# Kernel tuning notes

Measured on AMD Instinct MI355X. Metric: run time of the kernel, lower is better.

Reference implementation:

```python
import jax, jax.numpy as jnp
import numpy as np

B, N, K = 16, 1024, 20
EPS = 1e-5

def _lin_init(key, fan_in, fan_out):
    k1, k2 = jax.random.split(key)
    s = 1.0 / np.sqrt(fan_in)
    W = jax.random.uniform(k1, (fan_in, fan_out), minval=-s, maxval=s, dtype=jnp.float32)
    b = jax.random.uniform(k2, (fan_out,), minval=-s, maxval=s, dtype=jnp.float32)
    return W, b

def setup_inputs() -> dict:
    key = jax.random.key(0)
    ks = jax.random.split(key, 12)
    pos = jax.random.normal(ks[0], (B * N, 3), dtype=jnp.float32)
    batch = jnp.repeat(jnp.arange(B, dtype=jnp.int64), N)
    W1a, b1a = _lin_init(ks[1], 6, 64);    W1b, b1b = _lin_init(ks[2], 64, 64)
    W2a, b2a = _lin_init(ks[3], 128, 64);  W2b, b2b = _lin_init(ks[4], 64, 64)
    W3a, b3a = _lin_init(ks[5], 128, 128); W3b, b3b = _lin_init(ks[6], 128, 128)
    W4a, b4a = _lin_init(ks[7], 256, 256); W4b, b4b = _lin_init(ks[8], 256, 256)
    lin1_w, lin1_b = _lin_init(ks[9], 512, 1024)
    gamma = jnp.ones((1024,), jnp.float32); beta = jnp.zeros((1024,), jnp.float32)
    lin2_w, lin2_b = _lin_init(ks[10], 1024, 40)
    return dict(pos=pos, batch=batch,
                W1a=W1a, b1a=b1a, W1b=W1b, b1b=b1b,
                W2a=W2a, b2a=b2a, W2b=W2b, b2b=b2b,
                W3a=W3a, b3a=b3a, W3b=W3b, b3b=b3b,
                W4a=W4a, b4a=b4a, W4b=W4b, b4b=b4b,
                lin1_w=lin1_w, lin1_b=lin1_b, gamma=gamma, beta=beta,
                lin2_w=lin2_w, lin2_b=lin2_b)

def _edge_conv(x, Wa, ba, Wb, bb):
    # x: [B, N, C]. Dynamic kNN in feature space (per cloud, self included,
    # matching PyG knn), edge feature [x_i, x_j - x_i], MLP, max-aggregate.
    sq = jnp.sum(x * x, axis=-1)                                   # [B,N]
    d = sq[:, :, None] - 2.0 * jnp.einsum('bnc,bmc->bnm', x, x) + sq[:, None, :]
    _, idx = jax.lax.top_k(-d, K)                                  # [B,N,K]
    xj = jax.vmap(lambda xb, ib: xb[ib])(x, idx)                   # [B,N,K,C]
    xi = jnp.broadcast_to(x[:, :, None, :], xj.shape)
    e = jnp.concatenate([xi, xj - xi], axis=-1)                    # [B,N,K,2C]
    h = jax.nn.relu(e @ Wa + ba) @ Wb + bb                         # [B,N,K,Co]
    return jnp.max(h, axis=2)                                      # [B,N,Co]

def reference(pos, batch, W1a, b1a, W1b, b1b, W2a, b2a, W2b, b2b,
              W3a, b3a, W3b, b3b, W4a, b4a, W4b, b4b,
              lin1_w, lin1_b, gamma, beta, lin2_w, lin2_b):
    del batch  # clouds are equal-sized: batch == repeat(arange(B), N)
    x = pos.reshape(B, N, 3)
    x1 = _edge_conv(x,  W1a, b1a, W1b, b1b)   # [B,N,64]
    x2 = _edge_conv(x1, W2a, b2a, W2b, b2b)   # [B,N,64]
    x3 = _edge_conv(x2, W3a, b3a, W3b, b3b)   # [B,N,128]
    x4 = _edge_conv(x3, W4a, b4a, W4b, b4b)   # [B,N,256]
    x_cat = jnp.concatenate([x1, x2, x3, x4], axis=-1)  # [B,N,512]
    pooled = jnp.max(x_cat, axis=1)                      # global_max_pool -> [B,512]
    h = pooled @ lin1_w + lin1_b                         # [B,1024]
    mu = jnp.mean(h, axis=0)
    var = jnp.mean((h - mu) ** 2, axis=0)                # biased, as PyTorch BN
    h = (h - mu) * jax.lax.rsqrt(var + EPS) * gamma + beta
    h = jax.nn.relu(h)                                   # dropout is identity in eval
    logits = h @ lin2_w + lin2_b                         # [B,40]
    return jax.nn.log_softmax(logits, axis=1)
```

## Files before the change

kernel.cpp:

```cpp
#include <hip/hip_runtime.h>
#include <hip/hip_bf16.h>
#include <hip/hip_fp16.h>

#define B_   16
#define N_   1024
#define KNN  20
#define NP   (B_ * N_)

typedef short bf16x8 __attribute__((ext_vector_type(8)));
typedef _Float16 half8 __attribute__((ext_vector_type(8)));
typedef float f32x4  __attribute__((ext_vector_type(4)));
typedef float f32x16 __attribute__((ext_vector_type(16)));

__device__ __forceinline__ unsigned short f2bf(float f) {
  unsigned u = __float_as_uint(f);
  u += 0x7fffu + ((u >> 16) & 1u);
  return (unsigned short)(u >> 16);
}

__global__ __launch_bounds__(256) void pairdist_kernel(
    const float* __restrict__ X, int LD, int coff, int C,
    unsigned* __restrict__ Dk) {
  __shared__ __align__(16) char pd_smem[64 * 68 * 4];
  __shared__ float sqi_s[64], sqj_s[64];
  float (*Xi)[68] = (float(*)[68])pd_smem;
  float (*Xj)[68] = (float(*)[68])(pd_smem + 32 * 68 * 4);
  unsigned (*Tt)[68] = (unsigned(*)[68])pd_smem;
  int lin = blockIdx.x, by = 0;
  while (lin >= 16 - by) { lin -= 16 - by; ++by; }
  int bx = by + lin;
  int b  = blockIdx.z;
  int i0 = by * 64, j0 = bx * 64;
  int t  = threadIdx.x;
  int tx = t & 15, ty = t >> 4;
  int cx = t & 31, ry = t >> 5;
  float acc[4][4] = {};
  float sqacc = 0.f;
  for (int c0 = 0; c0 < C; c0 += 32) {
    int cc = min(32, C - c0);
    if (cx < cc) {
      for (int r = ry; r < 64; r += 8) {
        Xi[cx][r] = X[(size_t)(b * N_ + i0 + r) * LD + coff + c0 + cx];
        Xj[cx][r] = X[(size_t)(b * N_ + j0 + r) * LD + coff + c0 + cx];
      }
    }
    __syncthreads();
    if (t < 64) {
      for (int c = 0; c < cc; ++c) sqacc = fmaf(Xi[c][t], Xi[c][t], sqacc);
    } else if (t < 128) {
      int r = t - 64;
      for (int c = 0; c < cc; ++c) sqacc = fmaf(Xj[c][r], Xj[c][r], sqacc);
    }
    for (int c = 0; c < cc; ++c) {
      float4 a4 = *(const float4*)&Xi[c][ty * 4];
      float4 b4 = *(const float4*)&Xj[c][tx * 4];
      float a[4] = {a4.x, a4.y, a4.z, a4.w};
      float bb[4] = {b4.x, b4.y, b4.z, b4.w};
#pragma unroll
      for (int p = 0; p < 4; ++p)
#pragma unroll
        for (int q = 0; q < 4; ++q)
          acc[p][q] = fmaf(a[p], bb[q], acc[p][q]);
    }
    __syncthreads();
  }
  if (t < 64) sqi_s[t] = sqacc;
  else if (t < 128) sqj_s[t - 64] = sqacc;
  __syncthreads();
  float sqi[4], sqj[4];
#pragma unroll
  for (int p = 0; p < 4; ++p) sqi[p] = sqi_s[ty * 4 + p];
#pragma unroll
  for (int q = 0; q < 4; ++q) sqj[q] = sqj_s[tx * 4 + q];
  bool offdiag = (bx > by);
#pragma unroll
  for (int p = 0; p < 4; ++p) {
    uint4 st;
    unsigned* kk = (unsigned*)&st;
#pragma unroll
    for (int q = 0; q < 4; ++q) {
      float d = fmaxf((sqi[p] - 2.f * acc[p][q]) + sqj[q], 0.f);
      unsigned db = __float_as_uint(d) & 0xFFFFFC00u;
      kk[q] = db | (unsigned)(j0 + tx * 4 + q);
      if (offdiag)
        Tt[tx * 4 + q][ty * 4 + p] = db | (unsigned)(i0 + ty * 4 + p);
    }
    *(uint4*)&Dk[(size_t)(b * N_ + i0 + ty * 4 + p) * N_ + j0 + tx * 4] = st;
  }
  if (offdiag) {
    __syncthreads();
#pragma unroll
    for (int p = 0; p < 4; ++p) {
      *(uint4*)&Dk[(size_t)(b * N_ + j0 + ty * 4 + p) * N_ + i0 + tx * 4] =
          *(uint4*)&Tt[ty * 4 + p][tx * 4];
    }
  }
}

template<int C>
__global__ __launch_bounds__(256) void sqc_kernel(
    const float* __restrict__ X, int coff, float* __restrict__ sq) {
  int w = threadIdx.x >> 6, lane = threadIdx.x & 63;
  int pt = blockIdx.x * 4 + w;
  const float* xr = X + (size_t)pt * 512 + coff;
  float s = 0.f;
  for (int c = lane; c < C; c += 64) s = fmaf(xr[c], xr[c], s);
#pragma unroll
  for (int off = 32; off >= 1; off >>= 1) s += __shfl_xor(s, off);
  if (lane == 0) sq[pt] = s;
}

template<int C>
__global__ __launch_bounds__(256) void gramt_kernel(
    const float* __restrict__ X, int coff, const float* __restrict__ sqv,
    unsigned* __restrict__ Dk) {
  constexpr int KP = C / 64;
  __shared__ __align__(16) char gt_smem[32768];
  unsigned short* Phi = (unsigned short*)gt_smem;
  unsigned short* Plo = Phi + 4096;
  unsigned short* Qhi = Plo + 4096;
  unsigned short* Qlo = Qhi + 4096;
  unsigned (*Tt)[68] = (unsigned(*)[68])gt_smem;
  int tid = threadIdx.x, wv = tid >> 6, lane = tid & 63;
  int rc = lane & 31, half = lane >> 5;
  int lin = blockIdx.x, ti = 0;
  while (lin >= 16 - ti) { lin -= 16 - ti; ++ti; }
  int tj = ti + lin;
  int b  = blockIdx.z;
  int qi = wv >> 1, qj = wv & 1;
  f32x16 acc = {};
#pragma unroll
  for (int kp = 0; kp < KP; ++kp) {
    if (kp) __syncthreads();
#pragma unroll
    for (int it = 0; it < 4; ++it) {
      int u = tid + it * 256;
      int side = u >> 9;
      int row  = (u >> 3) & 63;
      int slot = u & 7;
      int grow = b * N_ + (side ? tj : ti) * 64 + row;
      const float* xr = X + (size_t)grow * 512 + coff + kp * 64 + slot * 8;
      float4 x0 = *(const float4*)xr;
      float4 x1 = *(const float4*)(xr + 4);
      float xs[8] = {x0.x, x0.y, x0.z, x0.w, x1.x, x1.y, x1.z, x1.w};
      union { half8 v; _Float16 h[8]; } H, L;
#pragma unroll
      for (int q = 0; q < 8; ++q) {
        _Float16 hv = (_Float16)xs[q];
        H.h[q] = hv;
        L.h[q] = (_Float16)(xs[q] - (float)hv);
      }
      int off = row * 64 + (slot ^ (row & 7)) * 8;
      if (side) { *(half8*)&Qhi[off] = H.v; *(half8*)&Qlo[off] = L.v; }
      else      { *(half8*)&Phi[off] = H.v; *(half8*)&Plo[off] = L.v; }
    }
    __syncthreads();
#pragma unroll
    for (int ch = 0; ch < 4; ++ch) {
      int s = ch * 2 + half;
      int arow = qi * 32 + rc, brow = qj * 32 + rc;
      int aoff = arow * 64 + (s ^ (arow & 7)) * 8;
      int boff = brow * 64 + (s ^ (brow & 7)) * 8;
      half8 Ah = *(const half8*)&Phi[aoff];
      half8 Al = *(const half8*)&Plo[aoff];
      half8 Bh = *(const half8*)&Qhi[boff];
      half8 Bl = *(const half8*)&Qlo[boff];
      acc = __builtin_amdgcn_mfma_f32_32x32x16_f16(Ah, Bh, acc, 0, 0, 0);
      acc = __builtin_amdgcn_mfma_f32_32x32x16_f16(Al, Bh, acc, 0, 0, 0);
      acc = __builtin_amdgcn_mfma_f32_32x32x16_f16(Ah, Bl, acc, 0, 0, 0);
    }
  }
  __syncthreads();
  bool offdiag = (tj > ti);
  int gj = tj * 64 + qj * 32 + rc;
  float sqj = sqv[b * N_ + gj];
#pragma unroll
  for (int e = 0; e < 16; ++e) {
    int erow = (e & 3) + 8 * (e >> 2) + 4 * half;
    int gi = ti * 64 + qi * 32 + erow;
    float sqi = sqv[b * N_ + gi];
    float d = fmaxf(sqi - 2.f * acc[e] + sqj, 0.f);
    if (gi == gj) d = 0.f;
    unsigned db = __float_as_uint(d) & 0xFFFFFC00u;
    Dk[(size_t)(b * N_ + gi) * N_ + gj] = db | (unsigned)gj;
    if (offdiag)
      Tt[qj * 32 + rc][qi * 32 + erow] = db | (unsigned)gi;
  }
  if (offdiag) {
    __syncthreads();
#pragma unroll
    for (int it = 0; it < 4; ++it) {
      int u = tid + it * 256;
      int r  = u >> 4;
      int c4 = (u & 15) * 4;
      uint4 vv = *(const uint4*)&Tt[r][c4];
      *(uint4*)&Dk[(size_t)(b * N_ + tj * 64 + r) * N_ + ti * 64 + c4] = vv;
    }
  }
}

__device__ __forceinline__ unsigned wave_min_bcast(unsigned x) {
  unsigned t;
  t = (unsigned)__builtin_amdgcn_update_dpp(-1, (int)x, 0x111, 0xF, 0xF, false);
  x = min(x, t);
  t = (unsigned)__builtin_amdgcn_update_dpp(-1, (int)x, 0x112, 0xF, 0xF, false);
  x = min(x, t);
  t = (unsigned)__builtin_amdgcn_update_dpp(-1, (int)x, 0x114, 0xF, 0xF, false);
  x = min(x, t);
  t = (unsigned)__builtin_amdgcn_update_dpp(-1, (int)x, 0x118, 0xF, 0xF, false);
  x = min(x, t);
  t = (unsigned)__builtin_amdgcn_update_dpp(-1, (int)x, 0x142, 0xF, 0xF, false);
  x = min(x, t);
  t = (unsigned)__builtin_amdgcn_update_dpp(-1, (int)x, 0x143, 0xF, 0xF, false);
  x = min(x, t);
  return (unsigned)__builtin_amdgcn_readlane((int)x, 63);
}

__global__ __launch_bounds__(256) void topk_kernel(
    const unsigned* __restrict__ Dk, int* __restrict__ idx) {
  int w = threadIdx.x >> 6, lane = threadIdx.x & 63;
  int p = blockIdx.x * 4 + w;
  const unsigned* row = Dk + (size_t)p * N_;
  unsigned key[16];
#pragma unroll
  for (int s = 0; s < 16; ++s) key[s] = row[lane + 64 * s];
  int base = p & ~(N_ - 1);
  for (int k = 0; k < KNN; ++k) {
    unsigned m = key[0];
#pragma unroll
    for (int s = 1; s < 16; ++s) m = min(m, key[s]);
    unsigned gm = wave_min_bcast(m);
    int j = (int)(gm & 1023u);
    if (lane == 0) idx[p * KNN + k] = base + j;
    if ((j & 63) == lane) key[j >> 6] = 0xFFFFFFFFu;
  }
}

__global__ __launch_bounds__(256) void transform_kernel(
    const float* __restrict__ X, int LD, int coff, int Cin, int Cmid,
    const float* __restrict__ Wa, const float* __restrict__ ba,
    unsigned short* __restrict__ u, unsigned short* __restrict__ v) {
  __shared__ float xs[16 * 128];
  int w = threadIdx.x >> 6, lane = threadIdx.x & 63;
  int m  = blockIdx.y * 64 + lane;
  int p0 = blockIdx.x * 16;
  for (int i = threadIdx.x; i < 16 * Cin; i += 256) {
    int pt = i / Cin, c = i - pt * Cin;
    xs[pt * Cin + c] = X[(size_t)(p0 + pt) * LD + coff + c];
  }
  __syncthreads();
  const float* xw = xs + (w * 4) * Cin;
  float ua[4] = {0.f, 0.f, 0.f, 0.f}, va[4] = {0.f, 0.f, 0.f, 0.f};
  for (int c = 0; c < Cin; ++c) {
    float wt = Wa[(size_t)c * Cmid + m];
    float wb = Wa[(size_t)(Cin + c) * Cmid + m];
    float wd = wt - wb;
#pragma unroll
    for (int i = 0; i < 4; ++i) {
      float xv = xw[i * Cin + c];
      ua[i] = fmaf(xv, wd, ua[i]);
      va[i] = fmaf(xv, wb, va[i]);
    }
  }
  float bias = ba[m];
#pragma unroll
  for (int i = 0; i < 4; ++i) {
    u[(size_t)(p0 + w * 4 + i) * Cmid + m] = f2bf(ua[i] + bias);
    v[(size_t)(p0 + w * 4 + i) * Cmid + m] = f2bf(va[i]);
  }
}

__global__ __launch_bounds__(256) void cvtwa_swz_kernel(
    const float* __restrict__ A2, const float* __restrict__ A3,
    const float* __restrict__ A4,
    unsigned short* __restrict__ d2, unsigned short* __restrict__ b2,
    unsigned short* __restrict__ d3, unsigned short* __restrict__ b3,
    unsigned short* __restrict__ d4, unsigned short* __restrict__ b4) {
  int z = blockIdx.z;
  const float* Wa; unsigned short *wd, *wb; int Cin, Cmid;
  if (z == 0)      { Wa = A2; wd = d2; wb = b2; Cin = 64;  Cmid = 64;  }
  else if (z == 1) { Wa = A3; wd = d3; wb = b3; Cin = 64;  Cmid = 128; }
  else             { Wa = A4; wd = d4; wb = b4; Cin = 128; Cmid = 256; }
  int KC = Cin / 16;
  int NC = (Cmid / 32) * KC * 64;
  int ci = blockIdx.x * 256 + threadIdx.x;
  if (ci >= NC) return;
  int ntc = ci >> 6, lane = ci & 63;
  int nt = ntc / KC, c = ntc - nt * KC;
  int n  = nt * 32 + (lane & 31);
  int kb = c * 16 + (lane >> 5) * 8;
#pragma unroll
  for (int j = 0; j < 8; ++j) {
    float top = Wa[(size_t)(kb + j) * Cmid + n];
    float bot = Wa[(size_t)(Cin + kb + j) * Cmid + n];
    wd[(size_t)ci * 8 + j] = f2bf(top - bot);
    wb[(size_t)ci * 8 + j] = f2bf(bot);
  }
}

template<int Cin, int Cmid>
__global__ __launch_bounds__(256) void transform_mfma_kernel(
    const float* __restrict__ X, int LD, int coff,
    const unsigned short* __restrict__ wdf, const unsigned short* __restrict__ wbf,
    const float* __restrict__ ba,
    unsigned short* __restrict__ u, unsigned short* __restrict__ v) {
  constexpr int KC = Cin / 16;
  int wv = threadIdx.x >> 6, lane = threadIdx.x & 63;
  int row = lane & 31, half = lane >> 5;
  int p0 = blockIdx.x * 128 + wv * 32;
  int nt = blockIdx.y;

  bf16x8 afr[KC];
  const float* xr = X + (size_t)(p0 + row) * LD + coff + half * 8;
#pragma unroll
  for (int c = 0; c < KC; ++c) {
    float4 x0 = *(const float4*)(xr + c * 16);
    float4 x1 = *(const float4*)(xr + c * 16 + 4);
    union { bf16x8 vec; __hip_bfloat162 h[4]; } pk;
    pk.h[0] = __float22bfloat162_rn({x0.x, x0.y});
    pk.h[1] = __float22bfloat162_rn({x0.z, x0.w});
    pk.h[2] = __float22bfloat162_rn({x1.x, x1.y});
    pk.h[3] = __float22bfloat162_rn({x1.z, x1.w});
    afr[c] = pk.vec;
  }

  const unsigned short* wdl = wdf + ((size_t)nt * KC * 64 + lane) * 8;
  const unsigned short* wbl = wbf + ((size_t)nt * KC * 64 + lane) * 8;
  f32x16 au = {}, av = {};
#pragma unroll
  for (int c = 0; c < KC; ++c) {
    bf16x8 bd = *(const bf16x8*)(wdl + (size_t)c * 512);
    au = __builtin_amdgcn_mfma_f32_32x32x16_bf16(afr[c], bd, au, 0, 0, 0);
  }
#pragma unroll
  for (int c = 0; c < KC; ++c) {
    bf16x8 bv = *(const bf16x8*)(wbl + (size_t)c * 512);
    av = __builtin_amdgcn_mfma_f32_32x32x16_bf16(afr[c], bv, av, 0, 0, 0);
  }

  int m = nt * 32 + row;
  float bias = ba[m];
#pragma unroll
  for (int e = 0; e < 16; ++e) {
    int orow = (e & 3) + 8 * (e >> 2) + 4 * half;
    u[(size_t)(p0 + orow) * Cmid + m] = f2bf(au[e] + bias);
    v[(size_t)(p0 + orow) * Cmid + m] = f2bf(av[e]);
  }
}

__global__ __launch_bounds__(256) void cvtw4_kernel(
    const float* __restrict__ W0, const float* __restrict__ W1,
    const float* __restrict__ W2, const float* __restrict__ W3,
    unsigned short* __restrict__ o0, unsigned short* __restrict__ o1,
    unsigned short* __restrict__ o2, unsigned short* __restrict__ o3) {
  __shared__ unsigned short tile[32][33];
  int z = blockIdx.z;
  const float* W; unsigned short* out; int Cmid, Cout;
  if (z == 0)      { W = W0; out = o0; Cmid = 64;  Cout = 64;  }
  else if (z == 1) { W = W1; out = o1; Cmid = 64;  Cout = 64;  }
  else if (z == 2) { W = W2; out = o2; Cmid = 128; Cout = 128; }
  else             { W = W3; out = o3; Cmid = 256; Cout = 256; }
  int c0 = blockIdx.x * 32, co0 = blockIdx.y * 32;
  if (c0 >= Cmid || co0 >= Cout) return;
  int tx = threadIdx.x & 31, ty = threadIdx.x >> 5;
  for (int r = ty; r < 32; r += 8)
    tile[r][tx] = f2bf(W[(size_t)(c0 + r) * Cout + co0 + tx]);
  __syncthreads();
  for (int r = ty; r < 32; r += 8)
    out[(size_t)(co0 + r) * Cmid + c0 + tx] = tile[tx][r];
}

template<int Cmid, int Cout, int CG>
__global__ __launch_bounds__(960, 3) void edge_mlp_kernel(
    const unsigned short* __restrict__ u, const unsigned short* __restrict__ v,
    const int* __restrict__ idx,
    const unsigned short* __restrict__ wbt, const float* __restrict__ bb,
    float* __restrict__ xcat, int coff) {
  constexpr int AP = Cmid + 8;
  constexpr int T  = CG / 32;
  constexpr int KC = Cmid / 16;
  constexpr int G  = Cout / CG;
  __shared__ __align__(16) unsigned short W_lds[CG * AP];
  __shared__ float qmax[120 * CG];
  int tid = threadIdx.x, w = tid >> 6, lane = tid & 63;
  int col = lane & 31, half = lane >> 5;

  int rg = blockIdx.x * 480 + w * 32 + col;
  int rgc = min(rg, NP * KNN - 1);
  int p  = rgc / 20;
  int j  = idx[rgc];
  const unsigned short* up = u + (size_t)p * Cmid + half * 8;
  const unsigned short* vp = v + (size_t)j * Cmid + half * 8;

  bf16x8 afr[KC];
#pragma unroll
  for (int c = 0; c < KC; ++c) {
    union { int4 i; __hip_bfloat162 h[4]; bf16x8 vec; } U, V, R;
    U.i = *(const int4*)(up + c * 16);
    V.i = *(const int4*)(vp + c * 16);
#pragma unroll
    for (int q = 0; q < 4; ++q) {
      float2 a = __bfloat1622float2(U.h[q]);
      float2 b = __bfloat1622float2(V.h[q]);
      R.h[q] = __float22bfloat162_rn({fmaxf(a.x + b.x, 0.f), fmaxf(a.y + b.y, 0.f)});
    }
    afr[c] = R.vec;
  }

  int brow = col * AP + half * 8;

  for (int g = 0; g < G; ++g) {
    __syncthreads();
    for (int i = tid; i < CG * (Cmid / 8); i += 960) {
      int rr = i / (Cmid / 8), q = i - rr * (Cmid / 8);
      *(int4*)&W_lds[rr * AP + q * 8] =
          *(const int4*)&wbt[(size_t)(g * CG + rr) * Cmid + q * 8];
    }
    __syncthreads();
    f32x16 acc[T] = {};
#pragma unroll
    for (int c = 0; c < KC; ++c) {
#pragma unroll
      for (int t = 0; t < T; ++t) {
        bf16x8 bf = *(const bf16x8*)&W_lds[brow + t * 32 * AP + c * 16];
        acc[t] = __builtin_amdgcn_mfma_f32_32x32x16_bf16(afr[c], bf, acc[t], 0, 0, 0);
      }
    }
#pragma unroll
    for (int t = 0; t < T; ++t) {
#pragma unroll
      for (int Q = 0; Q < 4; ++Q) {
        float m0 = fmaxf(fmaxf(acc[t][4 * Q], acc[t][4 * Q + 1]),
                         fmaxf(acc[t][4 * Q + 2], acc[t][4 * Q + 3]));
        qmax[(w * 8 + 2 * Q + half) * CG + t * 32 + col] = m0;
      }
    }
    __syncthreads();
    for (int i = tid; i < 24 * CG; i += 960) {
      int pl = i / CG, c2 = i - pl * CG;
      int pg = blockIdx.x * 24 + pl;
      if (pg < NP) {
        float mm = qmax[(pl * 5 + 0) * CG + c2];
#pragma unroll
        for (int qq = 1; qq < 5; ++qq) mm = fmaxf(mm, qmax[(pl * 5 + qq) * CG + c2]);
        xcat[(size_t)pg * 512 + coff + g * CG + c2] = mm + bb[g * CG + c2];
      }
    }
  }
}

__global__ __launch_bounds__(256) void pool1_kernel(const float* __restrict__ xcat,
                                                    float* __restrict__ part) {
  int b = blockIdx.x, g = blockIdx.y, t = threadIdx.x;
  const float* base = xcat + ((size_t)b * N_ + g * 128) * 512 + t * 2;
  float mx = -__builtin_inff(), my = -__builtin_inff();
#pragma unroll 4
  for (int r = 0; r < 128; ++r) {
    float2 vv = *(const float2*)(base + (size_t)r * 512);
    mx = fmaxf(mx, vv.x);
    my = fmaxf(my, vv.y);
  }
  *(float2*)&part[((size_t)b * 8 + g) * 512 + t * 2] = make_float2(mx, my);
}

__global__ __launch_bounds__(256) void pool2_kernel(const float* __restrict__ part,
                                                    float* __restrict__ pooled) {
  int b = blockIdx.x, t = threadIdx.x;
  float2 m = *(const float2*)&part[(size_t)b * 8 * 512 + t * 2];
#pragma unroll
  for (int g = 1; g < 8; ++g) {
    float2 vv = *(const float2*)&part[((size_t)b * 8 + g) * 512 + t * 2];
    m.x = fmaxf(m.x, vv.x);
    m.y = fmaxf(m.y, vv.y);
  }
  *(float2*)&pooled[b * 512 + t * 2] = m;
}

__global__ __launch_bounds__(256) void lin1_kernel(const float* __restrict__ pooled,
                                                   const float* __restrict__ W,
                                                   const float* __restrict__ bias,
                                                   float* __restrict__ h) {
  int flat = blockIdx.x * 256 + threadIdx.x;
  int b = flat >> 10, m = flat & 1023;
  float s = 0.f;
  for (int c = 0; c < 512; ++c) s = fmaf(pooled[b * 512 + c], W[(size_t)c * 1024 + m], s);
  h[flat] = s + bias[m];
}

__global__ __launch_bounds__(256) void bn_kernel(const float* __restrict__ h,
                                                 const float* __restrict__ gamma,
                                                 const float* __restrict__ beta,
                                                 float* __restrict__ h2) {
  int m = blockIdx.x * 256 + threadIdx.x;
  float s = 0.f;
  for (int b = 0; b < 16; ++b) s += h[b * 1024 + m];
  float mu = s * (1.f / 16.f);
  float vv = 0.f;
  for (int b = 0; b < 16; ++b) { float d = h[b * 1024 + m] - mu; vv = fmaf(d, d, vv); }
  vv *= (1.f / 16.f);
  float rstd = rsqrtf(vv + 1e-5f);
  float g = gamma[m] * rstd, be = beta[m];
  for (int b = 0; b < 16; ++b) {
    float val = (h[b * 1024 + m] - mu) * g + be;
    h2[b * 1024 + m] = fmaxf(val, 0.f);
  }
}

__global__ __launch_bounds__(64) void lin2_kernel(const float* __restrict__ h2,
                                                  const float* __restrict__ W,
                                                  const float* __restrict__ bias,
                                                  float* __restrict__ out) {
  int b = blockIdx.x, lane = threadIdx.x;
  float logit = 0.f;
  if (lane < 40) {
    logit = bias[lane];
    for (int c = 0; c < 1024; ++c)
      logit = fmaf(h2[b * 1024 + c], W[(size_t)c * 40 + lane], logit);
  }
  float mv = (lane < 40) ? logit : -__builtin_inff();
#pragma unroll
  for (int off = 32; off >= 1; off >>= 1) mv = fmaxf(mv, __shfl_xor(mv, off));
  float e = (lane < 40) ? expf(logit - mv) : 0.f;
#pragma unroll
  for (int off = 32; off >= 1; off >>= 1) e += __shfl_xor(e, off);
  float lse = mv + logf(e);
  if (lane < 40) out[b * 40 + lane] = logit - lse;
}

extern "C" void kernel_launch(void* const* d_in, const int* in_sizes, int n_in,
                              void* d_out, int out_size, void* d_ws, size_t ws_size,
                              hipStream_t stream) {
  const float* pos    = (const float*)d_in[0];
  const float* W1a = (const float*)d_in[2];  const float* b1a = (const float*)d_in[3];
  const float* W1b = (const float*)d_in[4];  const float* b1b = (const float*)d_in[5];
  const float* W2a = (const float*)d_in[6];  const float* b2a = (const float*)d_in[7];
  const float* W2b = (const float*)d_in[8];  const float* b2b = (const float*)d_in[9];
  const float* W3a = (const float*)d_in[10]; const float* b3a = (const float*)d_in[11];
  const float* W3b = (const float*)d_in[12]; const float* b3b = (const float*)d_in[13];
  const float* W4a = (const float*)d_in[14]; const float* b4a = (const float*)d_in[15];
  const float* W4b = (const float*)d_in[16]; const float* b4b = (const float*)d_in[17];
  const float* lin1_w = (const float*)d_in[18]; const float* lin1_b = (const float*)d_in[19];
  const float* gamma  = (const float*)d_in[20]; const float* beta   = (const float*)d_in[21];
  const float* lin2_w = (const float*)d_in[22]; const float* lin2_b = (const float*)d_in[23];
  float* out = (float*)d_out;

  char* ws = (char*)d_ws;
  size_t off = 0;
  auto alloc = [&](size_t bytes) {
    void* p = ws + off; off += (bytes + 255) & ~(size_t)255; return p;
  };
  float*    xcat = (float*)alloc((size_t)NP * 512 * 4);
  unsigned* Dk   = (unsigned*)alloc((size_t)NP * N_ * 4);
  int*      idx  = (int*)alloc((size_t)NP * KNN * 4);
  unsigned short* wbt1 = (unsigned short*)alloc(64 * 64 * 2);
  unsigned short* wbt2 = (unsigned short*)alloc(64 * 64 * 2);
  unsigned short* wbt3 = (unsigned short*)alloc(128 * 128 * 2);
  unsigned short* wbt4 = (unsigned short*)alloc(256 * 256 * 2);
  unsigned short* wd2 = (unsigned short*)alloc(64 * 64 * 2);
  unsigned short* wb2 = (unsigned short*)alloc(64 * 64 * 2);
  unsigned short* wd3 = (unsigned short*)alloc(64 * 128 * 2);
  unsigned short* wb3 = (unsigned short*)alloc(64 * 128 * 2);
  unsigned short* wd4 = (unsigned short*)alloc(128 * 256 * 2);
  unsigned short* wb4 = (unsigned short*)alloc(128 * 256 * 2);
  float* h      = (float*)alloc(16 * 1024 * 4);
  float* h2     = (float*)alloc(16 * 1024 * 4);
  float* pooled = (float*)alloc(16 * 512 * 4);
  float* part   = (float*)alloc(16 * 8 * 512 * 4);
  float* sqv    = (float*)alloc((size_t)NP * 4);
  unsigned short* u = (unsigned short*)Dk;
  unsigned short* v = (unsigned short*)Dk + (size_t)NP * 256;

  cvtw4_kernel<<<dim3(8, 8, 4), 256, 0, stream>>>(W1b, W2b, W3b, W4b,
                                                  wbt1, wbt2, wbt3, wbt4);
  cvtwa_swz_kernel<<<dim3(16, 1, 3), 256, 0, stream>>>(W2a, W3a, W4a,
                                                       wd2, wb2, wd3, wb3, wd4, wb4);

  dim3 pd_grid(136, 1, 16);
  dim3 gt_grid(136, 1, 16);
  const int EB = (NP * KNN + 479) / 480;
  pairdist_kernel<<<pd_grid, 256, 0, stream>>>(pos, 3, 0, 3, Dk);
  topk_kernel<<<NP / 4, 256, 0, stream>>>(Dk, idx);
  transform_kernel<<<dim3(NP / 16, 1), 256, 0, stream>>>(pos, 3, 0, 3, 64, W1a, b1a, u, v);
  edge_mlp_kernel<64, 64, 64><<<EB, 960, 0, stream>>>(u, v, idx, wbt1, b1b, xcat, 0);
  sqc_kernel<64><<<NP / 4, 256, 0, stream>>>(xcat, 0, sqv);
  gramt_kernel<64><<<gt_grid, 256, 0, stream>>>(xcat, 0, sqv, Dk);
  topk_kernel<<<NP / 4, 256, 0, stream>>>(Dk, idx);
  transform_mfma_kernel<64, 64><<<dim3(NP / 128, 2), 256, 0, stream>>>(
      xcat, 512, 0, wd2, wb2, b2a, u, v);
  edge_mlp_kernel<64, 64, 64><<<EB, 960, 0, stream>>>(u, v, idx, wbt2, b2b, xcat, 64);
  sqc_kernel<64><<<NP / 4, 256, 0, stream>>>(xcat, 64, sqv);
  gramt_kernel<64><<<gt_grid, 256, 0, stream>>>(xcat, 64, sqv, Dk);
  topk_kernel<<<NP / 4, 256, 0, stream>>>(Dk, idx);
  transform_mfma_kernel<64, 128><<<dim3(NP / 128, 4), 256, 0, stream>>>(
      xcat, 512, 64, wd3, wb3, b3a, u, v);
  edge_mlp_kernel<128, 128, 64><<<EB, 960, 0, stream>>>(u, v, idx, wbt3, b3b, xcat, 128);
  sqc_kernel<128><<<NP / 4, 256, 0, stream>>>(xcat, 128, sqv);
  gramt_kernel<128><<<gt_grid, 256, 0, stream>>>(xcat, 128, sqv, Dk);
  topk_kernel<<<NP / 4, 256, 0, stream>>>(Dk, idx);
  transform_mfma_kernel<128, 256><<<dim3(NP / 128, 8), 256, 0, stream>>>(
      xcat, 512, 128, wd4, wb4, b4a, u, v);
  edge_mlp_kernel<256, 256, 64><<<EB, 960, 0, stream>>>(u, v, idx, wbt4, b4b, xcat, 256);
  pool1_kernel<<<dim3(16, 8), 256, 0, stream>>>(xcat, part);
  pool2_kernel<<<16, 256, 0, stream>>>(part, pooled);
  lin1_kernel<<<64, 256, 0, stream>>>(pooled, lin1_w, lin1_b, h);
  bn_kernel<<<4, 256, 0, stream>>>(h, gamma, beta, h2);
  lin2_kernel<<<16, 64, 0, stream>>>(h2, lin2_w, lin2_b, out);
}
```

Measured before the change: 541.3 us.

## Fuse norm computation into gram kernel, merge weight converts, loop N-tiles in transform

Computes per-row squared norms inside the gram kernel via shared-memory atomics during tile staging, which removes three sqc kernel launches and the sqv buffer. Merges the two weight-conversion kernels into one launch. Changes transform_mfma to loop over all output column tiles within a block, so the A fragments are loaded once instead of once per tile. The trade-off is fewer blocks in the transform kernel and LDS atomic contention in the gram kernel.

```diff
diff --git a/kernel.cpp b/kernel.cpp
--- a/kernel.cpp
+++ b/kernel.cpp
@@ -98,22 +98,8 @@
 }
 
 template<int C>
-__global__ __launch_bounds__(256) void sqc_kernel(
-    const float* __restrict__ X, int coff, float* __restrict__ sq) {
-  int w = threadIdx.x >> 6, lane = threadIdx.x & 63;
-  int pt = blockIdx.x * 4 + w;
-  const float* xr = X + (size_t)pt * 512 + coff;
-  float s = 0.f;
-  for (int c = lane; c < C; c += 64) s = fmaf(xr[c], xr[c], s);
-#pragma unroll
-  for (int off = 32; off >= 1; off >>= 1) s += __shfl_xor(s, off);
-  if (lane == 0) sq[pt] = s;
-}
-
-template<int C>
 __global__ __launch_bounds__(256) void gramt_kernel(
-    const float* __restrict__ X, int coff, const float* __restrict__ sqv,
-    unsigned* __restrict__ Dk) {
+    const float* __restrict__ X, int coff, unsigned* __restrict__ Dk) {
   constexpr int KP = C / 64;
   __shared__ __align__(16) char gt_smem[32768];
   unsigned short* Phi = (unsigned short*)gt_smem;
@@ -121,6 +107,7 @@
   unsigned short* Qhi = Plo + 4096;
   unsigned short* Qlo = Qhi + 4096;
   unsigned (*Tt)[68] = (unsigned(*)[68])gt_smem;
+  __shared__ float nrmI[64], nrmJ[64];
   int tid = threadIdx.x, wv = tid >> 6, lane = tid & 63;
   int rc = lane & 31, half = lane >> 5;
   int lin = blockIdx.x, ti = 0;
@@ -128,6 +115,9 @@
   int tj = ti + lin;
   int b  = blockIdx.z;
   int qi = wv >> 1, qj = wv & 1;
+  if (tid < 64) nrmI[tid] = 0.f;
+  else if (tid < 128) nrmJ[tid - 64] = 0.f;
+  __syncthreads();
   f32x16 acc = {};
 #pragma unroll
   for (int kp = 0; kp < KP; ++kp) {
@@ -143,13 +133,16 @@
       float4 x0 = *(const float4*)xr;
       float4 x1 = *(const float4*)(xr + 4);
       float xs[8] = {x0.x, x0.y, x0.z, x0.w, x1.x, x1.y, x1.z, x1.w};
+      float ss = 0.f;
       union { half8 v; _Float16 h[8]; } H, L;
 #pragma unroll
       for (int q = 0; q < 8; ++q) {
+        ss = fmaf(xs[q], xs[q], ss);
         _Float16 hv = (_Float16)xs[q];
         H.h[q] = hv;
         L.h[q] = (_Float16)(xs[q] - (float)hv);
       }
+      atomicAdd(side ? &nrmJ[row] : &nrmI[row], ss);
       int off = row * 64 + (slot ^ (row & 7)) * 8;
       if (side) { *(half8*)&Qhi[off] = H.v; *(half8*)&Qlo[off] = L.v; }
       else      { *(half8*)&Phi[off] = H.v; *(half8*)&Plo[off] = L.v; }
@@ -173,12 +166,12 @@
   __syncthreads();
   bool offdiag = (tj > ti);
   int gj = tj * 64 + qj * 32 + rc;
-  float sqj = sqv[b * N_ + gj];
+  float sqj = nrmJ[qj * 32 + rc];
 #pragma unroll
   for (int e = 0; e < 16; ++e) {
     int erow = (e & 3) + 8 * (e >> 2) + 4 * half;
     int gi = ti * 64 + qi * 32 + erow;
-    float sqi = sqv[b * N_ + gi];
+    float sqi = nrmI[qi * 32 + erow];
     float d = fmaxf(sqi - 2.f * acc[e] + sqj, 0.f);
     if (gi == gj) d = 0.f;
     unsigned db = __float_as_uint(d) & 0xFFFFFC00u;
@@ -270,31 +263,54 @@
   }
 }
 
-__global__ __launch_bounds__(256) void cvtwa_swz_kernel(
+__global__ __launch_bounds__(256) void cvtall_kernel(
+    const float* __restrict__ W0, const float* __restrict__ W1,
+    const float* __restrict__ W2, const float* __restrict__ W3,
+    unsigned short* __restrict__ o0, unsigned short* __restrict__ o1,
+    unsigned short* __restrict__ o2, unsigned short* __restrict__ o3,
     const float* __restrict__ A2, const float* __restrict__ A3,
     const float* __restrict__ A4,
     unsigned short* __restrict__ d2, unsigned short* __restrict__ b2,
     unsigned short* __restrict__ d3, unsigned short* __restrict__ b3,
     unsigned short* __restrict__ d4, unsigned short* __restrict__ b4) {
   int z = blockIdx.z;
-  const float* Wa; unsigned short *wd, *wb; int Cin, Cmid;
-  if (z == 0)      { Wa = A2; wd = d2; wb = b2; Cin = 64;  Cmid = 64;  }
-  else if (z == 1) { Wa = A3; wd = d3; wb = b3; Cin = 64;  Cmid = 128; }
-  else             { Wa = A4; wd = d4; wb = b4; Cin = 128; Cmid = 256; }
-  int KC = Cin / 16;
-  int NC = (Cmid / 32) * KC * 64;
-  int ci = blockIdx.x * 256 + threadIdx.x;
-  if (ci >= NC) return;
-  int ntc = ci >> 6, lane = ci & 63;
-  int nt = ntc / KC, c = ntc - nt * KC;
-  int n  = nt * 32 + (lane & 31);
-  int kb = c * 16 + (lane >> 5) * 8;
-#pragma unroll
-  for (int j = 0; j < 8; ++j) {
-    float top = Wa[(size_t)(kb + j) * Cmid + n];
-    float bot = Wa[(size_t)(Cin + kb + j) * Cmid + n];
-    wd[(size_t)ci * 8 + j] = f2bf(top - bot);
-    wb[(size_t)ci * 8 + j] = f2bf(bot);
+  if (z < 4) {
+    __shared__ unsigned short tile[32][33];
+    const float* W; unsigned short* out; int Cmid, Cout;
+    if (z == 0)      { W = W0; out = o0; Cmid = 64;  Cout = 64;  }
+    else if (z == 1) { W = W1; out = o1; Cmid = 64;  Cout = 64;  }
+    else if (z == 2) { W = W2; out = o2; Cmid = 128; Cout = 128; }
+    else             { W = W3; out = o3; Cmid = 256; Cout = 256; }
+    int c0 = blockIdx.x * 32, co0 = blockIdx.y * 32;
+    if (c0 >= Cmid || co0 >= Cout) return;
+    int tx = threadIdx.x & 31, ty = threadIdx.x >> 5;
+    for (int r = ty; r < 32; r += 8)
+      tile[r][tx] = f2bf(W[(size_t)(c0 + r) * Cout + co0 + tx]);
+    __syncthreads();
+    for (int r = ty; r < 32; r += 8)
+      out[(size_t)(co0 + r) * Cmid + c0 + tx] = tile[tx][r];
+  } else {
+    if (blockIdx.y > 0) return;
+    int zz = z - 4;
+    const float* Wa; unsigned short *wd, *wb; int Cin, Cmid;
+    if (zz == 0)      { Wa = A2; wd = d2; wb = b2; Cin = 64;  Cmid = 64;  }
+    else if (zz == 1) { Wa = A3; wd = d3; wb = b3; Cin = 64;  Cmid = 128; }
+    else              { Wa = A4; wd = d4; wb = b4; Cin = 128; Cmid = 256; }
+    int KC = Cin / 16;
+    int NC = (Cmid / 32) * KC * 64;
+    int ci = blockIdx.x * 256 + threadIdx.x;
+    if (ci >= NC) return;
+    int ntc = ci >> 6, lane = ci & 63;
+    int nt = ntc / KC, c = ntc - nt * KC;
+    int n  = nt * 32 + (lane & 31);
+    int kb = c * 16 + (lane >> 5) * 8;
+#pragma unroll
+    for (int j = 0; j < 8; ++j) {
+      float top = Wa[(size_t)(kb + j) * Cmid + n];
+      float bot = Wa[(size_t)(Cin + kb + j) * Cmid + n];
+      wd[(size_t)ci * 8 + j] = f2bf(top - bot);
+      wb[(size_t)ci * 8 + j] = f2bf(bot);
+    }
   }
 }
 
@@ -305,10 +321,10 @@
     const float* __restrict__ ba,
     unsigned short* __restrict__ u, unsigned short* __restrict__ v) {
   constexpr int KC = Cin / 16;
+  constexpr int NT = Cmid / 32;
   int wv = threadIdx.x >> 6, lane = threadIdx.x & 63;
   int row = lane & 31, half = lane >> 5;
   int p0 = blockIdx.x * 128 + wv * 32;
-  int nt = blockIdx.y;
 
   bf16x8 afr[KC];
   const float* xr = X + (size_t)(p0 + row) * LD + coff + half * 8;
@@ -324,50 +340,29 @@
     afr[c] = pk.vec;
   }
 
-  const unsigned short* wdl = wdf + ((size_t)nt * KC * 64 + lane) * 8;
-  const unsigned short* wbl = wbf + ((size_t)nt * KC * 64 + lane) * 8;
-  f32x16 au = {}, av = {};
-#pragma unroll
-  for (int c = 0; c < KC; ++c) {
-    bf16x8 bd = *(const bf16x8*)(wdl + (size_t)c * 512);
-    au = __builtin_amdgcn_mfma_f32_32x32x16_bf16(afr[c], bd, au, 0, 0, 0);
-  }
-#pragma unroll
-  for (int c = 0; c < KC; ++c) {
-    bf16x8 bv = *(const bf16x8*)(wbl + (size_t)c * 512);
-    av = __builtin_amdgcn_mfma_f32_32x32x16_bf16(afr[c], bv, av, 0, 0, 0);
-  }
-
-  int m = nt * 32 + row;
-  float bias = ba[m];
-#pragma unroll
-  for (int e = 0; e < 16; ++e) {
-    int orow = (e & 3) + 8 * (e >> 2) + 4 * half;
-    u[(size_t)(p0 + orow) * Cmid + m] = f2bf(au[e] + bias);
-    v[(size_t)(p0 + orow) * Cmid + m] = f2bf(av[e]);
-  }
-}
-
-__global__ __launch_bounds__(256) void cvtw4_kernel(
-    const float* __restrict__ W0, const float* __restrict__ W1,
-    const float* __restrict__ W2, const float* __restrict__ W3,
-    unsigned short* __restrict__ o0, unsigned short* __restrict__ o1,
-    unsigned short* __restrict__ o2, unsigned short* __restrict__ o3) {
-  __shared__ unsigned short tile[32][33];
-  int z = blockIdx.z;
-  const float* W; unsigned short* out; int Cmid, Cout;
-  if (z == 0)      { W = W0; out = o0; Cmid = 64;  Cout = 64;  }
-  else if (z == 1) { W = W1; out = o1; Cmid = 64;  Cout = 64;  }
-  else if (z == 2) { W = W2; out = o2; Cmid = 128; Cout = 128; }
-  else             { W = W3; out = o3; Cmid = 256; Cout = 256; }
-  int c0 = blockIdx.x * 32, co0 = blockIdx.y * 32;
-  if (c0 >= Cmid || co0 >= Cout) return;
-  int tx = threadIdx.x & 31, ty = threadIdx.x >> 5;
-  for (int r = ty; r < 32; r += 8)
-    tile[r][tx] = f2bf(W[(size_t)(c0 + r) * Cout + co0 + tx]);
-  __syncthreads();
-  for (int r = ty; r < 32; r += 8)
-    out[(size_t)(co0 + r) * Cmid + c0 + tx] = tile[tx][r];
+  for (int nt = 0; nt < NT; ++nt) {
+    const unsigned short* wdl = wdf + ((size_t)nt * KC * 64 + lane) * 8;
+    const unsigned short* wbl = wbf + ((size_t)nt * KC * 64 + lane) * 8;
+    f32x16 au = {}, av = {};
+#pragma unroll
+    for (int c = 0; c < KC; ++c) {
+      bf16x8 bd = *(const bf16x8*)(wdl + (size_t)c * 512);
+      au = __builtin_amdgcn_mfma_f32_32x32x16_bf16(afr[c], bd, au, 0, 0, 0);
+    }
+#pragma unroll
+    for (int c = 0; c < KC; ++c) {
+      bf16x8 bv = *(const bf16x8*)(wbl + (size_t)c * 512);
+      av = __builtin_amdgcn_mfma_f32_32x32x16_bf16(afr[c], bv, av, 0, 0, 0);
+    }
+    int m = nt * 32 + row;
+    float bias = ba[m];
+#pragma unroll
+    for (int e = 0; e < 16; ++e) {
+      int orow = (e & 3) + 8 * (e >> 2) + 4 * half;
+      u[(size_t)(p0 + orow) * Cmid + m] = f2bf(au[e] + bias);
+      v[(size_t)(p0 + orow) * Cmid + m] = f2bf(av[e]);
+    }
+  }
 }
 
 template<int Cmid, int Cout, int CG>
@@ -566,14 +561,12 @@
   float* h2     = (float*)alloc(16 * 1024 * 4);
   float* pooled = (float*)alloc(16 * 512 * 4);
   float* part   = (float*)alloc(16 * 8 * 512 * 4);
-  float* sqv    = (float*)alloc((size_t)NP * 4);
   unsigned short* u = (unsigned short*)Dk;
   unsigned short* v = (unsigned short*)Dk + (size_t)NP * 256;
 
-  cvtw4_kernel<<<dim3(8, 8, 4), 256, 0, stream>>>(W1b, W2b, W3b, W4b,
-                                                  wbt1, wbt2, wbt3, wbt4);
-  cvtwa_swz_kernel<<<dim3(16, 1, 3), 256, 0, stream>>>(W2a, W3a, W4a,
-                                                       wd2, wb2, wd3, wb3, wd4, wb4);
+  cvtall_kernel<<<dim3(16, 8, 7), 256, 0, stream>>>(
+      W1b, W2b, W3b, W4b, wbt1, wbt2, wbt3, wbt4,
+      W2a, W3a, W4a, wd2, wb2, wd3, wb3, wd4, wb4);
 
   dim3 pd_grid(136, 1, 16);
   dim3 gt_grid(136, 1, 16);
@@ -582,22 +575,19 @@
   topk_kernel<<<NP / 4, 256, 0, stream>>>(Dk, idx);
   transform_kernel<<<dim3(NP / 16, 1), 256, 0, stream>>>(pos, 3, 0, 3, 64, W1a, b1a, u, v);
   edge_mlp_kernel<64, 64, 64><<<EB, 960, 0, stream>>>(u, v, idx, wbt1, b1b, xcat, 0);
-  sqc_kernel<64><<<NP / 4, 256, 0, stream>>>(xcat, 0, sqv);
-  gramt_kernel<64><<<gt_grid, 256, 0, stream>>>(xcat, 0, sqv, Dk);
+  gramt_kernel<64><<<gt_grid, 256, 0, stream>>>(xcat, 0, Dk);
   topk_kernel<<<NP / 4, 256, 0, stream>>>(Dk, idx);
-  transform_mfma_kernel<64, 64><<<dim3(NP / 128, 2), 256, 0, stream>>>(
+  transform_mfma_kernel<64, 64><<<NP / 128, 256, 0, stream>>>(
       xcat, 512, 0, wd2, wb2, b2a, u, v);
   edge_mlp_kernel<64, 64, 64><<<EB, 960, 0, stream>>>(u, v, idx, wbt2, b2b, xcat, 64);
-  sqc_kernel<64><<<NP / 4, 256, 0, stream>>>(xcat, 64, sqv);
-  gramt_kernel<64><<<gt_grid, 256, 0, stream>>>(xcat, 64, sqv, Dk);
+  gramt_kernel<64><<<gt_grid, 256, 0, stream>>>(xcat, 64, Dk);
   topk_kernel<<<NP / 4, 256, 0, stream>>>(Dk, idx);
-  transform_mfma_kernel<64, 128><<<dim3(NP / 128, 4), 256, 0, stream>>>(
+  transform_mfma_kernel<64, 128><<<NP / 128, 256, 0, stream>>>(
       xcat, 512, 64, wd3, wb3, b3a, u, v);
   edge_mlp_kernel<128, 128, 64><<<EB, 960, 0, stream>>>(u, v, idx, wbt3, b3b, xcat, 128);
-  sqc_kernel<128><<<NP / 4, 256, 0, stream>>>(xcat, 128, sqv);
-  gramt_kernel<128><<<gt_grid, 256, 0, stream>>>(xcat, 128, sqv, Dk);
+  gramt_kernel<128><<<gt_grid, 256, 0, stream>>>(xcat, 128, Dk);
   topk_kernel<<<NP / 4, 256, 0, stream>>>(Dk, idx);
-  transform_mfma_kernel<128, 256><<<dim3(NP / 128, 8), 256, 0, stream>>>(
+  transform_mfma_kernel<128, 256><<<NP / 128, 256, 0, stream>>>(
       xcat, 512, 128, wd4, wb4, b4a, u, v);
   edge_mlp_kernel<256, 256, 64><<<EB, 960, 0, stream>>>(u, v, idx, wbt4, b4b, xcat, 256);
   pool1_kernel<<<dim3(16, 8), 256, 0, stream>>>(xcat, part);
```

After: 595.8 us. 10.1% more time.
